# Kernel tuning notes

Hardware: AMD Instinct MI355X
Metric: run time of the kernel (lower is better)

Reference implementation:

```python
import jax, jax.numpy as jnp
import numpy as np

B, T, D = 2, 2048, 1024   # batch, seq, d_model
E, K, H = 8, 2, 704       # routed experts, topk, expert hidden
SH = 704 * 2              # shared-expert hidden = moe_hidden * num_shared_experts
EPS = 1e-20               # topk_norm_epsilon
STD = 0.02                # init_weight_std


def setup_inputs() -> dict:
    key = jax.random.key(0)
    ks = jax.random.split(key, 8)
    return {
        "x":   jax.random.normal(ks[0], (B, T, D), jnp.float32),
        "Wg":  jax.random.normal(ks[1], (E, D), jnp.float32) * STD,   # router experts_weights
        "W1":  jax.random.normal(ks[2], (E, D, H), jnp.float32) * STD,  # gate proj per expert
        "W3":  jax.random.normal(ks[3], (E, D, H), jnp.float32) * STD,  # up proj per expert
        "W2":  jax.random.normal(ks[4], (E, H, D), jnp.float32) * STD,  # down proj per expert
        "Ws1": jax.random.normal(ks[5], (D, SH), jnp.float32) * STD,    # shared expert
        "Ws3": jax.random.normal(ks[6], (D, SH), jnp.float32) * STD,
        "Ws2": jax.random.normal(ks[7], (SH, D), jnp.float32) * STD,
    }


def reference(x, Wg, W1, W3, W2, Ws1, Ws3, Ws2):
    b, t, d = x.shape
    n = b * t
    xf = x.reshape(n, d)
    # softmax gating + topk + scatter back into dense [N,E] gate matrix
    gates = jax.nn.softmax(xf @ Wg.T, axis=-1)                      # [N,E]
    top_v, top_i = jax.lax.top_k(gates, K)                          # [N,K]
    masked = jnp.zeros_like(gates).at[jnp.arange(n)[:, None], top_i].set(top_v)
    masked = masked / (masked.sum(-1, keepdims=True) + EPS)         # normalized_moe_gates
    # per-expert SwiGLU FFN over all tokens, then gate-weighted combine
    h = jnp.einsum('nd,edh->enh', xf, W1)                           # [E,N,H]
    g = jnp.einsum('nd,edh->enh', xf, W3)
    y = jnp.einsum('enh,ehd->end', jax.nn.silu(h) * g, W2)          # [E,N,D]
    routed = jnp.einsum('ne,end->nd', masked, y)                    # combine
    shared = (jax.nn.silu(xf @ Ws1) * (xf @ Ws3)) @ Ws2             # shared experts
    return (routed + shared).reshape(b, t, d)
```

## Files before the change

### kernel.cpp

```cpp
#include <hip/hip_runtime.h>
#include <math.h>

typedef __bf16 bf16;
typedef __attribute__((ext_vector_type(8))) __bf16 bf16x8;
typedef __attribute__((ext_vector_type(4))) __bf16 bf16x4;
typedef __attribute__((ext_vector_type(4))) float f32x4;

#define NTOK 4096
#define DM   1024
#define NE   8
#define NEX  10
#define HE   704

#define OFF_CNT   0u
#define OFF_TOK   256u
#define OFF_WGT   131328u
#define OFF_XB    262400u
#define OFF_W1T   8651008u
#define OFF_W3T   20185344u
#define OFF_W2T   31719680u
#define OFF_WS1T  43254016u
#define OFF_WS3T  46137600u
#define OFF_WS2T  49021184u
#define OFF_ACT   51904768u
#define OFF_EIDS  74973440u
#define OFF_GW    74989824u

__device__ __forceinline__ void async_cp16(const bf16* g, bf16* l)
{
    __builtin_amdgcn_global_load_lds(
        (const __attribute__((address_space(1))) unsigned int*)g,
        (__attribute__((address_space(3))) unsigned int*)l, 16, 0, 0);
}

__global__ void cvt_x_kernel(const float* __restrict__ x, bf16* __restrict__ xb, int n4)
{
    int i = blockIdx.x * blockDim.x + threadIdx.x;
    if (i >= n4) return;
    float4 v = ((const float4*)x)[i];
    bf16x4 o;
    o[0] = (bf16)v.x; o[1] = (bf16)v.y; o[2] = (bf16)v.z; o[3] = (bf16)v.w;
    ((bf16x4*)xb)[i] = o;
}

__global__ __launch_bounds__(256) void transpose_all(
    const float* __restrict__ W1, const float* __restrict__ W3, const float* __restrict__ W2,
    const float* __restrict__ Ws1, const float* __restrict__ Ws3, const float* __restrict__ Ws2,
    bf16* __restrict__ w1t, bf16* __restrict__ w3t, bf16* __restrict__ w2t,
    bf16* __restrict__ ws1t, bf16* __restrict__ ws3t, bf16* __restrict__ ws2t)
{
    int id = blockIdx.x;
    const float* src; bf16* dst; int C, rt, ct, nkt;
    if (id < 5632)       { int t = id;         int e = t / 704, m = t % 704; C = 704;
                           src = W1 + (size_t)e * 1024 * 704;  dst = w1t + (size_t)e * 720896;
                           ct = m % 22; rt = m / 22; nkt = 32; }
    else if (id < 11264) { int t = id - 5632;  int e = t / 704, m = t % 704; C = 704;
                           src = W3 + (size_t)e * 1024 * 704;  dst = w3t + (size_t)e * 720896;
                           ct = m % 22; rt = m / 22; nkt = 32; }
    else if (id < 16896) { int t = id - 11264; int e = t / 704, m = t % 704; C = 1024;
                           src = W2 + (size_t)e * 704 * 1024;  dst = w2t + (size_t)e * 720896;
                           ct = m % 32; rt = m / 32; nkt = 22; }
    else if (id < 18304) { int t = id - 16896; C = 1408; src = Ws1;
                           ct = t % 44; rt = t / 44; nkt = 32;
                           int ep = (ct >= 22) ? 1 : 0; ct -= 22 * ep;
                           src += (size_t)704 * ep;
                           dst = ws1t + (size_t)ep * 720896; }
    else if (id < 19712) { int t = id - 18304; C = 1408; src = Ws3;
                           ct = t % 44; rt = t / 44; nkt = 32;
                           int ep = (ct >= 22) ? 1 : 0; ct -= 22 * ep;
                           src += (size_t)704 * ep;
                           dst = ws3t + (size_t)ep * 720896; }
    else                 { int t = id - 19712; C = 1024; src = Ws2;
                           ct = t % 32; rt = t / 32; nkt = 22;
                           int ep = (rt >= 22) ? 1 : 0; rt -= 22 * ep;
                           src += (size_t)704 * 1024 * ep;
                           dst = ws2t + (size_t)ep * 720896; }

    __shared__ float tl[32][33];
    int c0 = ct * 32, r0 = rt * 32;
    int row  = threadIdx.x >> 3;
    int col4 = (threadIdx.x & 7) * 4;
    float4 v = *(const float4*)&src[(size_t)(r0 + row) * C + c0 + col4];
    tl[row][col4 + 0] = v.x; tl[row][col4 + 1] = v.y;
    tl[row][col4 + 2] = v.z; tl[row][col4 + 3] = v.w;
    __syncthreads();
    int n  = c0 + row;
    int ng = n >> 4, nr = n & 15;
    int kt = rt;
    int cc = col4 >> 3, j = col4 & 7;
    bf16x4 o;
    o[0] = (bf16)tl[col4 + 0][row];
    o[1] = (bf16)tl[col4 + 1][row];
    o[2] = (bf16)tl[col4 + 2][row];
    o[3] = (bf16)tl[col4 + 3][row];
    *(bf16x4*)&dst[(size_t)(((ng * nkt + kt) << 9) + (((cc << 4) | nr) << 3) + j)] = o;
}

__global__ __launch_bounds__(256) void router_logits(
    const float* __restrict__ x, const float* __restrict__ Wg,
    int* __restrict__ eids, float2* __restrict__ gw)
{
    int n    = blockIdx.x * 4 + (threadIdx.x >> 6);
    int lane = threadIdx.x & 63;
    const float* xrow = x + (size_t)n * DM;
    float xr[16];
    #pragma unroll
    for (int j = 0; j < 16; j++) xr[j] = xrow[lane + 64 * j];
    float logit[NE];
    #pragma unroll
    for (int e = 0; e < NE; e++) {
        const float* wr = Wg + e * DM;
        float s = 0.f;
        #pragma unroll
        for (int j = 0; j < 16; j++) s += xr[j] * wr[lane + 64 * j];
        #pragma unroll
        for (int off = 32; off; off >>= 1) s += __shfl_xor(s, off, 64);
        logit[e] = s;
    }
    if (lane == 0) {
        int i0 = 0;
        #pragma unroll
        for (int e = 1; e < NE; e++) if (logit[e] > logit[i0]) i0 = e;
        int i1 = (i0 == 0) ? 1 : 0;
        #pragma unroll
        for (int e = 0; e < NE; e++) if (e != i0 && logit[e] > logit[i1]) i1 = e;
        float m = logit[0];
        #pragma unroll
        for (int e = 1; e < NE; e++) m = fmaxf(m, logit[e]);
        float denom = 0.f;
        #pragma unroll
        for (int e = 0; e < NE; e++) denom += expf(logit[e] - m);
        float g0 = expf(logit[i0] - m) / denom;
        float g1 = expf(logit[i1] - m) / denom;
        float inv = 1.f / (g0 + g1 + 1e-20f);
        eids[n] = i0 | (i1 << 16);
        gw[n] = make_float2(g0 * inv, g1 * inv);
    }
}

__global__ __launch_bounds__(128) void build_lists(
    const int* __restrict__ eids, const float2* __restrict__ gw,
    int* __restrict__ cnt, int* __restrict__ tok, float* __restrict__ wgt)
{
    __shared__ int lcnt[NE];
    __shared__ int gbase[NE];
    int t = threadIdx.x;
    int n = blockIdx.x * 128 + t;
    if (t < NE) lcnt[t] = 0;
    __syncthreads();
    int packed = eids[n];
    float2 w = gw[n];
    int e0 = packed & 0xffff, e1 = packed >> 16;
    int s0 = atomicAdd(&lcnt[e0], 1);
    int s1 = atomicAdd(&lcnt[e1], 1);
    __syncthreads();
    if (t < NE) gbase[t] = atomicAdd(&cnt[t], lcnt[t]);
    __syncthreads();
    int p0 = gbase[e0] + s0, p1 = gbase[e1] + s1;
    tok[e0 * NTOK + p0] = n; wgt[e0 * NTOK + p0] = w.x;
    tok[e1 * NTOK + p1] = n; wgt[e1 * NTOK + p1] = w.y;
}

__global__ void prefix_kernel(const int* __restrict__ cnt, int* __restrict__ pfx)
{
    if (threadIdx.x == 0) {
        int s = 0;
        for (int e = 0; e < NEX; e++) { pfx[e] = s; s += (e < NE) ? cnt[e] : NTOK; }
        pfx[NEX] = s;
    }
}


__global__ __launch_bounds__(256) void gemm1_swiglu(
    const bf16* __restrict__ xb,
    const bf16* __restrict__ w1t, const bf16* __restrict__ w3t,
    const bf16* __restrict__ ws1t, const bf16* __restrict__ ws3t,
    bf16* __restrict__ act,
    const int* __restrict__ cnt, const int* __restrict__ pfx, const int* __restrict__ tok)
{
    int e = blockIdx.z;
    int count = (e < NE) ? cnt[e] : NTOK;
    int m0 = blockIdx.y * 128;
    if (m0 >= count) return;
    int h0 = blockIdx.x * 64;
    int base = pfx[e];
    const bf16 *B1, *B3;
    if (e < NE) { B1 = w1t + (size_t)e * 720896;        B3 = w3t + (size_t)e * 720896; }
    else        { B1 = ws1t + (size_t)(e - NE) * 720896; B3 = ws3t + (size_t)(e - NE) * 720896; }
    const int* tlist = (e < NE) ? tok + e * NTOK : nullptr;

    __shared__ bf16 As[8 * 512];
    __shared__ bf16 B1s[4 * 512];
    __shared__ bf16 B3s[4 * 512];

    int tid = threadIdx.x, w = tid >> 6, lane = tid & 63;

    int r3 = lane >> 2;
    int cx = (lane & 3) ^ ((r3 >> 1) & 3);
    int sA0 = m0 + 32 * w + r3, sA1 = sA0 + 16;
    int rA0 = tlist ? (sA0 < count ? tlist[sA0] : 0) : (sA0 < count ? sA0 : 0);
    int rA1 = tlist ? (sA1 < count ? tlist[sA1] : 0) : (sA1 < count ? sA1 : 0);
    const bf16* ga0 = xb + (size_t)rA0 * DM + cx * 8;
    const bf16* ga1 = xb + (size_t)rA1 * DM + cx * 8;
    bf16* lA0 = As + (2 * w) * 512;
    bf16* lA1 = As + (2 * w + 1) * 512;
    const bf16* gb1 = B1 + ((size_t)((h0 >> 4) + w) * 32) * 512 + lane * 8;
    const bf16* gb3 = B3 + ((size_t)((h0 >> 4) + w) * 32) * 512 + lane * 8;
    bf16* lB1 = B1s + w * 512;
    bf16* lB3 = B3s + w * 512;

    int rl = lane & 15, ch = lane >> 4;
    int uA = 4 * rl + (ch ^ ((rl >> 1) & 3));
    int gA = (w & 1) * 4;
    int gB = (w >> 1) * 2;
    int wm = (w & 1) * 64, wn = (w >> 1) * 32;

    f32x4 acch[4][2], accg[4][2];
    #pragma unroll
    for (int i = 0; i < 4; i++)
        #pragma unroll
        for (int j = 0; j < 2; j++) {
            acch[i][j] = (f32x4){0.f, 0.f, 0.f, 0.f};
            accg[i][j] = (f32x4){0.f, 0.f, 0.f, 0.f};
        }

    for (int k0 = 0; k0 < DM; k0 += 32) {
        async_cp16(ga0, lA0);
        async_cp16(ga1, lA1);
        async_cp16(gb1, lB1);
        async_cp16(gb3, lB3);
        ga0 += 32; ga1 += 32; gb1 += 512; gb3 += 512;
        __syncthreads();
        bf16x8 af[4], b1f[2], b3f[2];
        #pragma unroll
        for (int i = 0; i < 4; i++) af[i] = *(const bf16x8*)(As + (gA + i) * 512 + uA * 8);
        #pragma unroll
        for (int j = 0; j < 2; j++) {
            b1f[j] = *(const bf16x8*)(B1s + (gB + j) * 512 + lane * 8);
            b3f[j] = *(const bf16x8*)(B3s + (gB + j) * 512 + lane * 8);
        }
        #pragma unroll
        for (int i = 0; i < 4; i++)
            #pragma unroll
            for (int j = 0; j < 2; j++) {
                acch[i][j] = __builtin_amdgcn_mfma_f32_16x16x32_bf16(af[i], b1f[j], acch[i][j], 0, 0, 0);
                accg[i][j] = __builtin_amdgcn_mfma_f32_16x16x32_bf16(af[i], b3f[j], accg[i][j], 0, 0, 0);
            }
        __syncthreads();
    }

    #pragma unroll
    for (int i = 0; i < 4; i++)
        #pragma unroll
        for (int j = 0; j < 2; j++)
            #pragma unroll
            for (int r = 0; r < 4; r++) {
                int row = wm + i * 16 + ch * 4 + r;
                int s2 = m0 + row;
                if (s2 < count) {
                    float hv = acch[i][j][r], gv = accg[i][j][r];
                    float a = hv / (1.f + expf(-hv)) * gv;
                    act[(size_t)(base + s2) * HE + h0 + wn + j * 16 + rl] = (bf16)a;
                }
            }
}

__global__ __launch_bounds__(256) void gemm2_combine(
    const bf16* __restrict__ act,
    const bf16* __restrict__ w2t, const bf16* __restrict__ ws2t,
    float* __restrict__ out,
    const int* __restrict__ cnt, const int* __restrict__ pfx,
    const int* __restrict__ tok, const float* __restrict__ wgt)
{
    int e = blockIdx.z;
    int count = (e < NE) ? cnt[e] : NTOK;
    int m0 = blockIdx.y * 128;
    if (m0 >= count) return;
    int d0 = blockIdx.x * 128;
    int base = pfx[e];
    const bf16* B = (e < NE) ? w2t + (size_t)e * 720896 : ws2t + (size_t)(e - NE) * 720896;
    const int*   tlist = (e < NE) ? tok + e * NTOK : nullptr;
    const float* wl    = (e < NE) ? wgt + e * NTOK : nullptr;

    __shared__ bf16 As[8 * 512];
    __shared__ bf16 Bs[8 * 512];

    int tid = threadIdx.x, w = tid >> 6, lane = tid & 63;

    int r3 = lane >> 2;
    int cx = (lane & 3) ^ ((r3 >> 1) & 3);
    int sA0 = m0 + 32 * w + r3, sA1 = sA0 + 16;
    int a0 = (sA0 < count) ? (base + sA0) : base;
    int a1 = (sA1 < count) ? (base + sA1) : base;
    const bf16* ga0 = act + (size_t)a0 * HE + cx * 8;
    const bf16* ga1 = act + (size_t)a1 * HE + cx * 8;
    bf16* lA0 = As + (2 * w) * 512;
    bf16* lA1 = As + (2 * w + 1) * 512;
    const bf16* gb0 = B + ((size_t)((d0 >> 4) + 2 * w) * 22) * 512 + lane * 8;
    const bf16* gb1 = B + ((size_t)((d0 >> 4) + 2 * w + 1) * 22) * 512 + lane * 8;
    bf16* lB0 = Bs + (2 * w) * 512;
    bf16* lB1 = Bs + (2 * w + 1) * 512;

    int rl = lane & 15, ch = lane >> 4;
    int uA = 4 * rl + (ch ^ ((rl >> 1) & 3));
    int gA = (w & 1) * 4, gB = (w >> 1) * 4;
    int wm = (w & 1) * 64, wn = (w >> 1) * 64;

    f32x4 acc[4][4];
    #pragma unroll
    for (int i = 0; i < 4; i++)
        #pragma unroll
        for (int j = 0; j < 4; j++) acc[i][j] = (f32x4){0.f, 0.f, 0.f, 0.f};

    for (int k0 = 0; k0 < HE; k0 += 32) {
        async_cp16(ga0, lA0);
        async_cp16(ga1, lA1);
        async_cp16(gb0, lB0);
        async_cp16(gb1, lB1);
        ga0 += 32; ga1 += 32; gb0 += 512; gb1 += 512;
        __syncthreads();
        bf16x8 af[4], bf_[4];
        #pragma unroll
        for (int i = 0; i < 4; i++) af[i]  = *(const bf16x8*)(As + (gA + i) * 512 + uA * 8);
        #pragma unroll
        for (int j = 0; j < 4; j++) bf_[j] = *(const bf16x8*)(Bs + (gB + j) * 512 + lane * 8);
        #pragma unroll
        for (int i = 0; i < 4; i++)
            #pragma unroll
            for (int j = 0; j < 4; j++)
                acc[i][j] = __builtin_amdgcn_mfma_f32_16x16x32_bf16(af[i], bf_[j], acc[i][j], 0, 0, 0);
        __syncthreads();
    }

    #pragma unroll
    for (int i = 0; i < 4; i++)
        #pragma unroll
        for (int j = 0; j < 4; j++)
            #pragma unroll
            for (int r = 0; r < 4; r++) {
                int row = wm + i * 16 + ch * 4 + r;
                int s2 = m0 + row;
                if (s2 < count) {
                    int   t  = tlist ? tlist[s2] : s2;
                    float wt = wl ? wl[s2] : 1.0f;
                    int col = d0 + wn + j * 16 + rl;
                    atomicAdd(&out[(size_t)t * DM + col], wt * acc[i][j][r]);
                }
            }
}

extern "C" void kernel_launch(void* const* d_in, const int* in_sizes, int n_in,
                              void* d_out, int out_size, void* d_ws, size_t ws_size,
                              hipStream_t stream)
{
    const float* x   = (const float*)d_in[0];
    const float* Wg  = (const float*)d_in[1];
    const float* W1  = (const float*)d_in[2];
    const float* W3  = (const float*)d_in[3];
    const float* W2  = (const float*)d_in[4];
    const float* Ws1 = (const float*)d_in[5];
    const float* Ws3 = (const float*)d_in[6];
    const float* Ws2 = (const float*)d_in[7];
    float* out = (float*)d_out;
    char*  ws  = (char*)d_ws;

    int*    cnt  = (int*)(ws + OFF_CNT);
    int*    pfx  = (int*)(ws + OFF_CNT + 32);
    int*    tok  = (int*)(ws + OFF_TOK);
    float*  wgt  = (float*)(ws + OFF_WGT);
    bf16*   xb   = (bf16*)(ws + OFF_XB);
    bf16*   w1t  = (bf16*)(ws + OFF_W1T);
    bf16*   w3t  = (bf16*)(ws + OFF_W3T);
    bf16*   w2t  = (bf16*)(ws + OFF_W2T);
    bf16*   ws1t = (bf16*)(ws + OFF_WS1T);
    bf16*   ws3t = (bf16*)(ws + OFF_WS3T);
    bf16*   ws2t = (bf16*)(ws + OFF_WS2T);
    bf16*   act  = (bf16*)(ws + OFF_ACT);
    int*    eids = (int*)(ws + OFF_EIDS);
    float2* gw   = (float2*)(ws + OFF_GW);

    hipMemsetAsync(ws, 0, 256, stream);
    hipMemsetAsync(out, 0, (size_t)NTOK * DM * sizeof(float), stream);

    cvt_x_kernel<<<4096, 256, 0, stream>>>(x, xb, NTOK * DM / 4);
    transpose_all<<<21120, 256, 0, stream>>>(W1, W3, W2, Ws1, Ws3, Ws2,
                                             w1t, w3t, w2t, ws1t, ws3t, ws2t);
    router_logits<<<1024, 256, 0, stream>>>(x, Wg, eids, gw);
    build_lists<<<32, 128, 0, stream>>>(eids, gw, cnt, tok, wgt);
    prefix_kernel<<<1, 64, 0, stream>>>(cnt, pfx);

    gemm1_swiglu<<<dim3(HE / 64, 32, NEX), 256, 0, stream>>>(
        xb, w1t, w3t, ws1t, ws3t, act, cnt, pfx, tok);
    gemm2_combine<<<dim3(DM / 128, 32, NEX), 256, 0, stream>>>(
        act, w2t, ws2t, out, cnt, pfx, tok, wgt);
}
```

Measured before the change: 344.8 us.

## Replace atomic combine with per-slot routed outputs, shared GEMM, and gather-add

Splits the second GEMM into a routed kernel that writes gate-weighted bf16 rows to a per-slot buffer and a shared-expert kernel that sums both shared halves in registers and stores to the output directly. A final gather kernel adds each token's two routed rows into the output using slot indices recorded during list building. This removes float atomics, the output memset, and the repeated accumulation from the shared halves. In exchange it adds an extra bf16 intermediate round trip through memory, an extra launch, and rounding of routed outputs to bf16 before accumulation.

```diff
diff --git a/kernel.cpp b/kernel.cpp
--- a/kernel.cpp
+++ b/kernel.cpp
@@ -25,6 +25,8 @@
 #define OFF_ACT   51904768u
 #define OFF_EIDS  74973440u
 #define OFF_GW    74989824u
+#define OFF_SLOT  75022592u
+#define OFF_YR    OFF_W1T
 
 __device__ __forceinline__ void async_cp16(const bf16* g, bf16* l)
 {
@@ -140,7 +142,8 @@
 
 __global__ __launch_bounds__(128) void build_lists(
     const int* __restrict__ eids, const float2* __restrict__ gw,
-    int* __restrict__ cnt, int* __restrict__ tok, float* __restrict__ wgt)
+    int* __restrict__ cnt, int* __restrict__ tok, float* __restrict__ wgt,
+    int2* __restrict__ slots)
 {
     __shared__ int lcnt[NE];
     __shared__ int gbase[NE];
@@ -159,6 +162,7 @@
     int p0 = gbase[e0] + s0, p1 = gbase[e1] + s1;
     tok[e0 * NTOK + p0] = n; wgt[e0 * NTOK + p0] = w.x;
     tok[e1 * NTOK + p1] = n; wgt[e1 * NTOK + p1] = w.y;
+    slots[n] = make_int2((e0 << 16) | p0, (e1 << 16) | p1);
 }
 
 __global__ void prefix_kernel(const int* __restrict__ cnt, int* __restrict__ pfx)
@@ -265,22 +269,21 @@
             }
 }
 
-__global__ __launch_bounds__(256) void gemm2_combine(
+__global__ __launch_bounds__(256) void gemm2_routed(
     const bf16* __restrict__ act,
-    const bf16* __restrict__ w2t, const bf16* __restrict__ ws2t,
-    float* __restrict__ out,
+    const bf16* __restrict__ w2t,
+    bf16* __restrict__ yr,
     const int* __restrict__ cnt, const int* __restrict__ pfx,
-    const int* __restrict__ tok, const float* __restrict__ wgt)
+    const float* __restrict__ wgt)
 {
     int e = blockIdx.z;
-    int count = (e < NE) ? cnt[e] : NTOK;
+    int count = cnt[e];
     int m0 = blockIdx.y * 128;
     if (m0 >= count) return;
     int d0 = blockIdx.x * 128;
     int base = pfx[e];
-    const bf16* B = (e < NE) ? w2t + (size_t)e * 720896 : ws2t + (size_t)(e - NE) * 720896;
-    const int*   tlist = (e < NE) ? tok + e * NTOK : nullptr;
-    const float* wl    = (e < NE) ? wgt + e * NTOK : nullptr;
+    const bf16* B = w2t + (size_t)e * 720896;
+    const float* wl = wgt + e * NTOK;
 
     __shared__ bf16 As[8 * 512];
     __shared__ bf16 Bs[8 * 512];
@@ -312,7 +315,7 @@
         #pragma unroll
         for (int j = 0; j < 4; j++) acc[i][j] = (f32x4){0.f, 0.f, 0.f, 0.f};
 
-    for (int k0 = 0; k0 < HE; k0 += 32) {
+    for (int kt = 0; kt < 22; kt++) {
         async_cp16(ga0, lA0);
         async_cp16(ga1, lA1);
         async_cp16(gb0, lB0);
@@ -333,20 +336,115 @@
     }
 
     #pragma unroll
+    for (int i = 0; i < 4; i++) {
+        #pragma unroll
+        for (int r = 0; r < 4; r++) {
+            int row = wm + i * 16 + ch * 4 + r;
+            int s2 = m0 + row;
+            if (s2 < count) {
+                float wt = wl[s2];
+                bf16* yrow = yr + (size_t)(base + s2) * DM + d0 + wn;
+                #pragma unroll
+                for (int j = 0; j < 4; j++)
+                    yrow[j * 16 + rl] = (bf16)(wt * acc[i][j][r]);
+            }
+        }
+    }
+}
+
+__global__ __launch_bounds__(256) void gemm2_shared(
+    const bf16* __restrict__ act,
+    const bf16* __restrict__ ws2t,
+    float* __restrict__ out)
+{
+    int m0 = blockIdx.y * 128;
+    int d0 = blockIdx.x * 128;
+
+    __shared__ bf16 As[8 * 512];
+    __shared__ bf16 Bs[8 * 512];
+
+    int tid = threadIdx.x, w = tid >> 6, lane = tid & 63;
+
+    int r3 = lane >> 2;
+    int cx = (lane & 3) ^ ((r3 >> 1) & 3);
+    int sA0 = m0 + 32 * w + r3, sA1 = sA0 + 16;
+    bf16* lA0 = As + (2 * w) * 512;
+    bf16* lA1 = As + (2 * w + 1) * 512;
+    bf16* lB0 = Bs + (2 * w) * 512;
+    bf16* lB1 = Bs + (2 * w + 1) * 512;
+
+    int rl = lane & 15, ch = lane >> 4;
+    int uA = 4 * rl + (ch ^ ((rl >> 1) & 3));
+    int gA = (w & 1) * 4, gB = (w >> 1) * 4;
+    int wm = (w & 1) * 64, wn = (w >> 1) * 64;
+
+    f32x4 acc[4][4];
+    #pragma unroll
     for (int i = 0; i < 4; i++)
         #pragma unroll
-        for (int j = 0; j < 4; j++)
-            #pragma unroll
-            for (int r = 0; r < 4; r++) {
-                int row = wm + i * 16 + ch * 4 + r;
-                int s2 = m0 + row;
-                if (s2 < count) {
-                    int   t  = tlist ? tlist[s2] : s2;
-                    float wt = wl ? wl[s2] : 1.0f;
-                    int col = d0 + wn + j * 16 + rl;
-                    atomicAdd(&out[(size_t)t * DM + col], wt * acc[i][j][r]);
-                }
-            }
+        for (int j = 0; j < 4; j++) acc[i][j] = (f32x4){0.f, 0.f, 0.f, 0.f};
+
+    #pragma unroll
+    for (int h = 0; h < 2; h++) {
+        int rowbase = 8192 + 4096 * h;
+        const bf16* ga0 = act + (size_t)(rowbase + sA0) * HE + cx * 8;
+        const bf16* ga1 = act + (size_t)(rowbase + sA1) * HE + cx * 8;
+        const bf16* B = ws2t + (size_t)h * 720896;
+        const bf16* gb0 = B + ((size_t)((d0 >> 4) + 2 * w) * 22) * 512 + lane * 8;
+        const bf16* gb1 = B + ((size_t)((d0 >> 4) + 2 * w + 1) * 22) * 512 + lane * 8;
+        for (int kt = 0; kt < 22; kt++) {
+            async_cp16(ga0, lA0);
+            async_cp16(ga1, lA1);
+            async_cp16(gb0, lB0);
+            async_cp16(gb1, lB1);
+            ga0 += 32; ga1 += 32; gb0 += 512; gb1 += 512;
+            __syncthreads();
+            bf16x8 af[4], bf_[4];
+            #pragma unroll
+            for (int i = 0; i < 4; i++) af[i]  = *(const bf16x8*)(As + (gA + i) * 512 + uA * 8);
+            #pragma unroll
+            for (int j = 0; j < 4; j++) bf_[j] = *(const bf16x8*)(Bs + (gB + j) * 512 + lane * 8);
+            #pragma unroll
+            for (int i = 0; i < 4; i++)
+                #pragma unroll
+                for (int j = 0; j < 4; j++)
+                    acc[i][j] = __builtin_amdgcn_mfma_f32_16x16x32_bf16(af[i], bf_[j], acc[i][j], 0, 0, 0);
+            __syncthreads();
+        }
+    }
+
+    #pragma unroll
+    for (int i = 0; i < 4; i++)
+        #pragma unroll
+        for (int r = 0; r < 4; r++) {
+            int row = wm + i * 16 + ch * 4 + r;
+            float* orow = out + (size_t)(m0 + row) * DM + d0 + wn;
+            #pragma unroll
+            for (int j = 0; j < 4; j++)
+                orow[j * 16 + rl] = acc[i][j][r];
+        }
+}
+
+__global__ __launch_bounds__(256) void fuse_add(
+    const bf16* __restrict__ yr, const int2* __restrict__ slots,
+    const int* __restrict__ pfx, float* __restrict__ out)
+{
+    int n = blockIdx.x;
+    int2 s = slots[n];
+    int slot0 = pfx[s.x >> 16] + (s.x & 0xffff);
+    int slot1 = pfx[s.y >> 16] + (s.y & 0xffff);
+    const bf16* y0 = yr + (size_t)slot0 * DM;
+    const bf16* y1 = yr + (size_t)slot1 * DM;
+    float* orow = out + (size_t)n * DM;
+    int d = threadIdx.x * 4;
+    bf16x4 a = *(const bf16x4*)(y0 + d);
+    bf16x4 b = *(const bf16x4*)(y1 + d);
+    float4 o = *(float4*)(orow + d);
+    o.x += (float)a[0] + (float)b[0];
+    o.y += (float)a[1] + (float)b[1];
+    o.z += (float)a[2] + (float)b[2];
+    o.w += (float)a[3] + (float)b[3];
+    *(float4*)(orow + d) = o;
 }
 
 extern "C" void kernel_launch(void* const* d_in, const int* in_sizes, int n_in,
@@ -364,33 +462,38 @@
     float* out = (float*)d_out;
     char*  ws  = (char*)d_ws;
 
-    int*    cnt  = (int*)(ws + OFF_CNT);
-    int*    pfx  = (int*)(ws + OFF_CNT + 32);
-    int*    tok  = (int*)(ws + OFF_TOK);
-    float*  wgt  = (float*)(ws + OFF_WGT);
-    bf16*   xb   = (bf16*)(ws + OFF_XB);
-    bf16*   w1t  = (bf16*)(ws + OFF_W1T);
-    bf16*   w3t  = (bf16*)(ws + OFF_W3T);
-    bf16*   w2t  = (bf16*)(ws + OFF_W2T);
-    bf16*   ws1t = (bf16*)(ws + OFF_WS1T);
-    bf16*   ws3t = (bf16*)(ws + OFF_WS3T);
-    bf16*   ws2t = (bf16*)(ws + OFF_WS2T);
-    bf16*   act  = (bf16*)(ws + OFF_ACT);
-    int*    eids = (int*)(ws + OFF_EIDS);
-    float2* gw   = (float2*)(ws + OFF_GW);
+    int*    cnt   = (int*)(ws + OFF_CNT);
+    int*    pfx   = (int*)(ws + OFF_CNT + 32);
+    int*    tok   = (int*)(ws + OFF_TOK);
+    float*  wgt   = (float*)(ws + OFF_WGT);
+    bf16*   xb    = (bf16*)(ws + OFF_XB);
+    bf16*   w1t   = (bf16*)(ws + OFF_W1T);
+    bf16*   w3t   = (bf16*)(ws + OFF_W3T);
+    bf16*   w2t   = (bf16*)(ws + OFF_W2T);
+    bf16*   ws1t  = (bf16*)(ws + OFF_WS1T);
+    bf16*   ws3t  = (bf16*)(ws + OFF_WS3T);
+    bf16*   ws2t  = (bf16*)(ws + OFF_WS2T);
+    bf16*   act   = (bf16*)(ws + OFF_ACT);
+    int*    eids  = (int*)(ws + OFF_EIDS);
+    float2* gw    = (float2*)(ws + OFF_GW);
+    int2*   slots = (int2*)(ws + OFF_SLOT);
+    bf16*   yr    = (bf16*)(ws + OFF_YR);
 
     hipMemsetAsync(ws, 0, 256, stream);
-    hipMemsetAsync(out, 0, (size_t)NTOK * DM * sizeof(float), stream);
 
     cvt_x_kernel<<<4096, 256, 0, stream>>>(x, xb, NTOK * DM / 4);
     transpose_all<<<21120, 256, 0, stream>>>(W1, W3, W2, Ws1, Ws3, Ws2,
                                              w1t, w3t, w2t, ws1t, ws3t, ws2t);
     router_logits<<<1024, 256, 0, stream>>>(x, Wg, eids, gw);
-    build_lists<<<32, 128, 0, stream>>>(eids, gw, cnt, tok, wgt);
+    build_lists<<<32, 128, 0, stream>>>(eids, gw, cnt, tok, wgt, slots);
     prefix_kernel<<<1, 64, 0, stream>>>(cnt, pfx);
 
     gemm1_swiglu<<<dim3(HE / 64, 32, NEX), 256, 0, stream>>>(
         xb, w1t, w3t, ws1t, ws3t, act, cnt, pfx, tok);
-    gemm2_combine<<<dim3(DM / 128, 32, NEX), 256, 0, stream>>>(
-        act, w2t, ws2t, out, cnt, pfx, tok, wgt);
-}
+
+    gemm2_routed<<<dim3(DM / 128, 32, NE), 256, 0, stream>>>(
+        act, w2t, yr, cnt, pfx, wgt);
+    gemm2_shared<<<dim3(DM / 128, NTOK / 128, 1), 256, 0, stream>>>(
+        act, ws2t, out);
+    fuse_add<<<NTOK, 256, 0, stream>>>(yr, slots, pfx, out);
+}
```

New measurement: 324.1 us. 6.0% less time.
